# Kernel optimization log

Measured on AMD Instinct MI355X. Metric: run time of the kernel, lower is better.

## Reference

```python
import jax, jax.numpy as jnp
import numpy as np

B, S, D_IN, D_OUT, E = 4, 2048, 1024, 1024, 8

def setup_inputs() -> dict:
    key = jax.random.key(0)
    ks = jax.random.split(key, 5)
    scale = 1.0 / np.sqrt(D_IN)
    x  = jax.random.normal(ks[0], (B, S, D_IN), dtype=jnp.float32)
    We = jax.random.uniform(ks[1], (E, D_OUT, D_IN), dtype=jnp.float32, minval=-scale, maxval=scale)
    be = jax.random.uniform(ks[2], (E, D_OUT), dtype=jnp.float32, minval=-scale, maxval=scale)
    Wg = jax.random.uniform(ks[3], (E, D_IN), dtype=jnp.float32, minval=-scale, maxval=scale)
    bg = jax.random.uniform(ks[4], (E,), dtype=jnp.float32, minval=-scale, maxval=scale)
    return {"x": x, "We": We, "be": be, "Wg": Wg, "bg": bg}

def reference(x, We, be, Wg, bg):
    # gate: [B,S,E]
    gate_logits = jnp.einsum('bsd,ed->bse', x, Wg) + bg
    gate = jax.nn.softmax(gate_logits, axis=-1)
    top1 = jnp.argmax(gate, axis=-1)                      # [B,S]
    one_hot = jax.nn.one_hot(top1, E, dtype=x.dtype)      # [B,S,E]
    # all-expert dense outputs, stacked on last axis: [B,S,O,E]
    expert_outs = jnp.einsum('bsd,eod->bsoe', x, We) + be.T
    out = jnp.einsum('bsoe,bse->bso', expert_outs, one_hot)
    mean_gate = gate.mean(axis=(0, 1))                    # [E]
    aux_loss = jnp.mean((mean_gate * E) ** 2)
    return (out, aux_loss)
```

## Files before the change

kernel.cpp:

```cpp
#include <hip/hip_runtime.h>
#include <hip/hip_bf16.h>


#define NTOK 8192
#define DIN  1024
#define DOUT 1024
#define NE   8

typedef unsigned short u16;
typedef unsigned int   u32;
typedef unsigned long long u64;
typedef short  bf16x8 __attribute__((ext_vector_type(8)));
typedef float  f32x4  __attribute__((ext_vector_type(4)));

__device__ __forceinline__ u16 f2bf(float f) {
    __hip_bfloat16 h = __float2bfloat16(f);
    return *(u16*)&h;
}


__global__ __launch_bounds__(256) void gate_kernel(
    const float* __restrict__ x, const float* __restrict__ Wg,
    const float* __restrict__ bg, u32* __restrict__ stage)
{
    __shared__ int   am_s[16];
    __shared__ float mg_s[4][NE];

    const int tid  = threadIdx.x;
    const int wave = tid >> 6;
    const int lane = tid & 63;
    const int g    = lane >> 3;
    const int sub  = lane & 7;

    const float* wr = Wg + g * DIN + 4 * sub;

    float bgl[NE];
    #pragma unroll
    for (int e = 0; e < NE; ++e) bgl[e] = bg[e];

    float mgacc = 0.f;

    #pragma unroll 1
    for (int it = 0; it < 4; ++it) {
        const int t = blockIdx.x * 16 + wave * 4 + it;
        const float* xr = x + (size_t)t * DIN + 4 * sub;

        float acc0 = 0.f, acc1 = 0.f, acc2 = 0.f, acc3 = 0.f;
        #pragma unroll
        for (int j = 0; j < 8; ++j) {
            const int k = j * 128;
            f32x4 x0 = *(const f32x4*)(xr + k);
            f32x4 w0 = *(const f32x4*)(wr + k);
            f32x4 x1 = *(const f32x4*)(xr + k + 32);
            f32x4 w1 = *(const f32x4*)(wr + k + 32);
            f32x4 x2 = *(const f32x4*)(xr + k + 64);
            f32x4 w2 = *(const f32x4*)(wr + k + 64);
            f32x4 x3 = *(const f32x4*)(xr + k + 96);
            f32x4 w3 = *(const f32x4*)(wr + k + 96);
            #pragma unroll
            for (int q = 0; q < 4; ++q) {
                acc0 = fmaf(w0[q], x0[q], acc0);
                acc1 = fmaf(w1[q], x1[q], acc1);
                acc2 = fmaf(w2[q], x2[q], acc2);
                acc3 = fmaf(w3[q], x3[q], acc3);
            }
        }
        float acc = (acc0 + acc1) + (acc2 + acc3);

        acc += __shfl_xor(acc, 1, 64);
        acc += __shfl_xor(acc, 2, 64);
        acc += __shfl_xor(acc, 4, 64);

        float logit[NE];
        #pragma unroll
        for (int e = 0; e < NE; ++e)
            logit[e] = __shfl(acc, e * 8, 64) + bgl[e];

        float m = logit[0]; int am = 0;
        #pragma unroll
        for (int e = 1; e < NE; ++e) if (logit[e] > m) { m = logit[e]; am = e; }

        float p[NE], s = 0.f;
        #pragma unroll
        for (int e = 0; e < NE; ++e) { p[e] = __expf(logit[e] - m); s += p[e]; }
        const float inv = 1.f / s;

        float psel = p[0];
        #pragma unroll
        for (int e = 1; e < NE; ++e) psel = (lane == e) ? p[e] : psel;
        if (lane < NE) mgacc += psel * inv;

        if (lane == 0) am_s[wave * 4 + it] = am;
    }

    if (lane < NE) mg_s[wave][lane] = mgacc;
    __syncthreads();

    u32* rec = stage + (size_t)blockIdx.x * 16;
    if (tid == 0) {
        u64 pack = 0;
        #pragma unroll
        for (int i = 0; i < 16; ++i) pack |= (u64)am_s[i] << (4 * i);
        *(u64*)rec = pack;
    }
    if (tid < NE) {
        float s = mg_s[0][tid] + mg_s[1][tid] + mg_s[2][tid] + mg_s[3][tid];
        rec[2 + tid] = __float_as_uint(s);
    }
}

__global__ __launch_bounds__(512) void route_kernel(
    const u32* __restrict__ stage, int* __restrict__ counts,
    int* __restrict__ tok_list, float* __restrict__ out)
{
    __shared__ float mgl[512][NE];
    __shared__ int   c[512][9];
    __shared__ float tot_s[NE];

    const int tid  = threadIdx.x;
    const int wave = tid >> 6;
    const int lane = tid & 63;

    const u64 pack = *(const u64*)(stage + (size_t)tid * 16);
    #pragma unroll
    for (int e = 0; e < NE; ++e)
        mgl[tid][e] = __uint_as_float(stage[tid * 16 + 2 + e]);

    #pragma unroll
    for (int e = 0; e < 9; ++e) c[tid][e] = 0;

    #pragma unroll
    for (int it = 0; it < 16; ++it) {
        int e3 = (int)((pack >> (4 * it)) & 7);
        c[tid][e3]++;
    }
    __syncthreads();

    {
        const int e = wave;
        int carry = 0;
        #pragma unroll 1
        for (int ch = 0; ch < 8; ++ch) {
            int v = c[ch * 64 + lane][e];
            int incl = v;
            #pragma unroll
            for (int off = 1; off < 64; off <<= 1) {
                int n = __shfl_up(incl, off, 64);
                if (lane >= off) incl += n;
            }
            c[ch * 64 + lane][e] = incl - v + carry;
            carry += __shfl(incl, 63, 64);
        }
        if (lane == 0) counts[e] = carry;
    }
    __syncthreads();

    #pragma unroll
    for (int it = 0; it < 16; ++it) {
        int e3 = (int)((pack >> (4 * it)) & 7);
        int pos = c[tid][e3]++;
        tok_list[e3 * NTOK + pos] = tid * 16 + it;
    }

    {
        const int e = wave;
        float s = 0.f;
        #pragma unroll
        for (int ch = 0; ch < 8; ++ch) s += mgl[ch * 64 + lane][e];
        #pragma unroll
        for (int off = 32; off > 0; off >>= 1) s += __shfl_xor(s, off, 64);
        if (lane == 0) tot_s[e] = s;
    }
    __syncthreads();
    if (tid == 0) {
        float s = 0.f;
        #pragma unroll
        for (int e = 0; e < NE; ++e) {
            float m = tot_s[e] * (8.0f / 8192.0f);
            s += m * m;
        }
        out[(size_t)NTOK * DOUT] = s * 0.125f;
    }
}

__global__ __launch_bounds__(256) void moe_gemm(
    const float* __restrict__ x, const float* __restrict__ We,
    const float* __restrict__ be, const int* __restrict__ counts,
    const int* __restrict__ tok_list, float* __restrict__ out)
{
    const int e   = blockIdx.z;
    const int cnt = counts[e];
    const int m0  = blockIdx.y * 128;
    if (m0 >= cnt) return;
    const int n0  = blockIdx.x * 128;

    __shared__ u16 sA[128 * 32];
    __shared__ u16 sB[128 * 32];
    __shared__ int toks[128];

    const int tid = threadIdx.x;
    if (tid < 128) {
        int gr = m0 + tid;
        toks[tid] = (gr < cnt) ? tok_list[e * NTOK + gr] : tok_list[e * NTOK];
    }
    __syncthreads();

    const int lane = tid & 63;
    const int wave = tid >> 6;
    const int wm   = (wave & 1) * 64;
    const int wn   = (wave >> 1) * 64;
    const int lrow = lane & 15;
    const int quad = lane >> 4;

    f32x4 acc[4][4];
    #pragma unroll
    for (int i = 0; i < 4; ++i)
        #pragma unroll
        for (int j = 0; j < 4; ++j) acc[i][j] = (f32x4){0.f, 0.f, 0.f, 0.f};

    const int srow  = tid >> 1;
    const int shalf = (tid & 1) * 16;

    const float* xrow = x  + (size_t)toks[srow] * DIN + shalf;
    const float* brow = We + ((size_t)e << 20) + ((size_t)(n0 + srow) << 10) + shalf;

    #pragma unroll 1
    for (int k0 = 0; k0 < DIN; k0 += 32) {
        f32x4 a[4], b[4];
        #pragma unroll
        for (int q = 0; q < 4; ++q) {
            a[q] = *(const f32x4*)(xrow + k0 + 4 * q);
            b[q] = *(const f32x4*)(brow + k0 + 4 * q);
        }
        union { u16 h[16]; uint4 u[2]; } pa, pb;
        #pragma unroll
        for (int q = 0; q < 4; ++q)
            #pragma unroll
            for (int j = 0; j < 4; ++j) {
                pa.h[q * 4 + j] = f2bf(a[q][j]);
                pb.h[q * 4 + j] = f2bf(b[q][j]);
            }
        *(uint4*)&sA[srow * 32 + shalf]     = pa.u[0];
        *(uint4*)&sA[srow * 32 + shalf + 8] = pa.u[1];
        *(uint4*)&sB[srow * 32 + shalf]     = pb.u[0];
        *(uint4*)&sB[srow * 32 + shalf + 8] = pb.u[1];
        __syncthreads();

        bf16x8 af[4], bfr[4];
        #pragma unroll
        for (int i = 0; i < 4; ++i)
            af[i] = *(const bf16x8*)&sA[(wm + i * 16 + lrow) * 32 + quad * 8];
        #pragma unroll
        for (int j = 0; j < 4; ++j)
            bfr[j] = *(const bf16x8*)&sB[(wn + j * 16 + lrow) * 32 + quad * 8];
        #pragma unroll
        for (int i = 0; i < 4; ++i)
            #pragma unroll
            for (int j = 0; j < 4; ++j)
                acc[i][j] = __builtin_amdgcn_mfma_f32_16x16x32_bf16(
                    af[i], bfr[j], acc[i][j], 0, 0, 0);
        __syncthreads();
    }

    #pragma unroll
    for (int j = 0; j < 4; ++j) {
        const int col = n0 + wn + j * 16 + lrow;
        const float bev = be[e * DOUT + col];
        #pragma unroll
        for (int i = 0; i < 4; ++i) {
            #pragma unroll
            for (int r = 0; r < 4; ++r) {
                const int rl = wm + i * 16 + quad * 4 + r;
                if (m0 + rl < cnt) {
                    const int tok = toks[rl];
                    out[((size_t)tok << 10) + col] = acc[i][j][r] + bev;
                }
            }
        }
    }
}

extern "C" void kernel_launch(void* const* d_in, const int* in_sizes, int n_in,
                              void* d_out, int out_size, void* d_ws, size_t ws_size,
                              hipStream_t stream) {
    const float* x  = (const float*)d_in[0];
    const float* We = (const float*)d_in[1];
    const float* be = (const float*)d_in[2];
    const float* Wg = (const float*)d_in[3];
    const float* bg = (const float*)d_in[4];
    float* out = (float*)d_out;

    int* counts   = (int*)d_ws;
    int* tok_list = (int*)((char*)d_ws + 256);
    u32* stage    = (u32*)((char*)d_ws + 256);

    gate_kernel<<<512, 256, 0, stream>>>(x, Wg, bg, stage);
    route_kernel<<<1, 512, 0, stream>>>(stage, counts, tok_list, out);
    moe_gemm<<<dim3(8, 64, 8), 256, 0, stream>>>(x, We, be, counts, tok_list, out);
}
```

Baseline: 187.0 us.

## Double K-tile to 64 with XOR-swizzled LDS and flattened expert-major grid

Result: slower. 276.2 us (+47.7%).

```diff
diff --git a/kernel.cpp b/kernel.cpp
--- a/kernel.cpp
+++ b/kernel.cpp
@@ -188,14 +188,15 @@
     const float* __restrict__ be, const int* __restrict__ counts,
     const int* __restrict__ tok_list, float* __restrict__ out)
 {
-    const int e   = blockIdx.z;
+    const int d  = blockIdx.x;
+    const int e  = (d >> 6) & 7;
     const int cnt = counts[e];
-    const int m0  = blockIdx.y * 128;
+    const int m0 = (d & 63) * 128;
     if (m0 >= cnt) return;
-    const int n0  = blockIdx.x * 128;
-
-    __shared__ u16 sA[128 * 32];
-    __shared__ u16 sB[128 * 32];
+    const int n0 = (d >> 9) * 128;
+
+    __shared__ u16 sA[128 * 64];
+    __shared__ u16 sB[128 * 64];
     __shared__ int toks[128];
 
     const int tid = threadIdx.x;
@@ -218,47 +219,65 @@
         #pragma unroll
         for (int j = 0; j < 4; ++j) acc[i][j] = (f32x4){0.f, 0.f, 0.f, 0.f};
 
-    const int srow  = tid >> 1;
-    const int shalf = (tid & 1) * 16;
-
-    const float* xrow = x  + (size_t)toks[srow] * DIN + shalf;
-    const float* brow = We + ((size_t)e << 20) + ((size_t)(n0 + srow) << 10) + shalf;
+    const int t3 = tid >> 3;
+    const int ch = tid & 7;
+    const int cx = ch ^ (t3 & 7);
+
+    const float* aP[4];
+    const float* bP[4];
+    #pragma unroll
+    for (int p = 0; p < 4; ++p) {
+        const int r = p * 32 + t3;
+        aP[p] = x  + (size_t)toks[r] * DIN + ch * 8;
+        bP[p] = We + ((size_t)e << 20) + ((size_t)(n0 + r) << 10) + ch * 8;
+    }
+
+    const int l7 = lrow & 7;
 
     #pragma unroll 1
-    for (int k0 = 0; k0 < DIN; k0 += 32) {
-        f32x4 a[4], b[4];
-        #pragma unroll
-        for (int q = 0; q < 4; ++q) {
-            a[q] = *(const f32x4*)(xrow + k0 + 4 * q);
-            b[q] = *(const f32x4*)(brow + k0 + 4 * q);
-        }
-        union { u16 h[16]; uint4 u[2]; } pa, pb;
-        #pragma unroll
-        for (int q = 0; q < 4; ++q)
-            #pragma unroll
-            for (int j = 0; j < 4; ++j) {
-                pa.h[q * 4 + j] = f2bf(a[q][j]);
-                pb.h[q * 4 + j] = f2bf(b[q][j]);
-            }
-        *(uint4*)&sA[srow * 32 + shalf]     = pa.u[0];
-        *(uint4*)&sA[srow * 32 + shalf + 8] = pa.u[1];
-        *(uint4*)&sB[srow * 32 + shalf]     = pb.u[0];
-        *(uint4*)&sB[srow * 32 + shalf + 8] = pb.u[1];
+    for (int k0 = 0; k0 < DIN; k0 += 64) {
+        f32x4 a0[4], a1[4], b0[4], b1[4];
+        #pragma unroll
+        for (int p = 0; p < 4; ++p) {
+            a0[p] = *(const f32x4*)(aP[p] + k0);
+            a1[p] = *(const f32x4*)(aP[p] + k0 + 4);
+            b0[p] = *(const f32x4*)(bP[p] + k0);
+            b1[p] = *(const f32x4*)(bP[p] + k0 + 4);
+        }
+        #pragma unroll
+        for (int p = 0; p < 4; ++p) {
+            union { u16 h[8]; uint4 u; } ua, ub;
+            #pragma unroll
+            for (int q = 0; q < 4; ++q) {
+                ua.h[q]     = f2bf(a0[p][q]);
+                ua.h[4 + q] = f2bf(a1[p][q]);
+                ub.h[q]     = f2bf(b0[p][q]);
+                ub.h[4 + q] = f2bf(b1[p][q]);
+            }
+            const int r = p * 32 + t3;
+            *(uint4*)&sA[r * 64 + cx * 8] = ua.u;
+            *(uint4*)&sB[r * 64 + cx * 8] = ub.u;
+        }
         __syncthreads();
 
-        bf16x8 af[4], bfr[4];
-        #pragma unroll
-        for (int i = 0; i < 4; ++i)
-            af[i] = *(const bf16x8*)&sA[(wm + i * 16 + lrow) * 32 + quad * 8];
-        #pragma unroll
-        for (int j = 0; j < 4; ++j)
-            bfr[j] = *(const bf16x8*)&sB[(wn + j * 16 + lrow) * 32 + quad * 8];
-        #pragma unroll
-        for (int i = 0; i < 4; ++i)
-            #pragma unroll
-            for (int j = 0; j < 4; ++j)
-                acc[i][j] = __builtin_amdgcn_mfma_f32_16x16x32_bf16(
-                    af[i], bfr[j], acc[i][j], 0, 0, 0);
+        bf16x8 af[2][4], bfr[2][4];
+        #pragma unroll
+        for (int ks = 0; ks < 2; ++ks) {
+            const int so = ((ks * 4 + quad) ^ l7) * 8;
+            #pragma unroll
+            for (int i = 0; i < 4; ++i) {
+                af[ks][i]  = *(const bf16x8*)&sA[(wm + i * 16 + lrow) * 64 + so];
+                bfr[ks][i] = *(const bf16x8*)&sB[(wn + i * 16 + lrow) * 64 + so];
+            }
+        }
+        #pragma unroll
+        for (int ks = 0; ks < 2; ++ks)
+            #pragma unroll
+            for (int i = 0; i < 4; ++i)
+                #pragma unroll
+                for (int j = 0; j < 4; ++j)
+                    acc[i][j] = __builtin_amdgcn_mfma_f32_16x16x32_bf16(
+                        af[ks][i], bfr[ks][j], acc[i][j], 0, 0, 0);
         __syncthreads();
     }
 
@@ -296,5 +315,5 @@
 
     gate_kernel<<<512, 256, 0, stream>>>(x, Wg, bg, stage);
     route_kernel<<<1, 512, 0, stream>>>(stage, counts, tok_list, out);
-    moe_gemm<<<dim3(8, 64, 8), 256, 0, stream>>>(x, We, be, counts, tok_list, out);
-}
+    moe_gemm<<<4096, 256, 0, stream>>>(x, We, be, counts, tok_list, out);
+}
```

## Replace LDS-staged GEMM with single-wave register-direct tiles and double-buffered loads

Applied to the files above, without the earlier changes.

Result: slower. 284.4 us (+52.1%).

```diff
diff --git a/kernel.cpp b/kernel.cpp
--- a/kernel.cpp
+++ b/kernel.cpp
@@ -183,98 +183,110 @@
     }
 }
 
-__global__ __launch_bounds__(256) void moe_gemm(
+__global__ __launch_bounds__(64) void moe_gemm(
     const float* __restrict__ x, const float* __restrict__ We,
     const float* __restrict__ be, const int* __restrict__ counts,
     const int* __restrict__ tok_list, float* __restrict__ out)
 {
-    const int e   = blockIdx.z;
+    const int d   = blockIdx.x;
+    const int mlo = d & 7;
+    const int n   = (d >> 3) & 15;
+    const int e   = (d >> 7) & 7;
+    const int mhi = d >> 10;
     const int cnt = counts[e];
-    const int m0  = blockIdx.y * 128;
+    const int m0  = (mlo + 8 * mhi) * 64;
     if (m0 >= cnt) return;
-    const int n0  = blockIdx.x * 128;
-
-    __shared__ u16 sA[128 * 32];
-    __shared__ u16 sB[128 * 32];
-    __shared__ int toks[128];
-
-    const int tid = threadIdx.x;
-    if (tid < 128) {
-        int gr = m0 + tid;
-        toks[tid] = (gr < cnt) ? tok_list[e * NTOK + gr] : tok_list[e * NTOK];
-    }
-    __syncthreads();
-
-    const int lane = tid & 63;
-    const int wave = tid >> 6;
-    const int wm   = (wave & 1) * 64;
-    const int wn   = (wave >> 1) * 64;
+    const int n0  = n * 64;
+
+    const int lane = threadIdx.x;
     const int lrow = lane & 15;
     const int quad = lane >> 4;
 
+    int atok[4];
+    #pragma unroll
+    for (int i = 0; i < 4; ++i) {
+        int gr = m0 + i * 16 + lrow;
+        atok[i] = tok_list[e * NTOK + (gr < cnt ? gr : cnt - 1)];
+    }
+
+    const float* aP[4];
+    const float* bP[4];
+    #pragma unroll
+    for (int i = 0; i < 4; ++i)
+        aP[i] = x + (size_t)atok[i] * DIN + quad * 8;
+    #pragma unroll
+    for (int j = 0; j < 4; ++j)
+        bP[j] = We + ((size_t)e << 20) + ((size_t)(n0 + j * 16 + lrow) << 10) + quad * 8;
+
     f32x4 acc[4][4];
     #pragma unroll
     for (int i = 0; i < 4; ++i)
         #pragma unroll
         for (int j = 0; j < 4; ++j) acc[i][j] = (f32x4){0.f, 0.f, 0.f, 0.f};
 
-    const int srow  = tid >> 1;
-    const int shalf = (tid & 1) * 16;
-
-    const float* xrow = x  + (size_t)toks[srow] * DIN + shalf;
-    const float* brow = We + ((size_t)e << 20) + ((size_t)(n0 + srow) << 10) + shalf;
-
+    f32x4 A0[8], B0[8], A1[8], B1[8];
+
+    #define LD(Ab, Bb, k0)                                       \
+        do {                                                     \
+            _Pragma("unroll")                                    \
+            for (int i = 0; i < 4; ++i) {                        \
+                Ab[2*i]   = *(const f32x4*)(aP[i] + (k0));       \
+                Ab[2*i+1] = *(const f32x4*)(aP[i] + (k0) + 4);   \
+                Bb[2*i]   = *(const f32x4*)(bP[i] + (k0));       \
+                Bb[2*i+1] = *(const f32x4*)(bP[i] + (k0) + 4);   \
+            }                                                    \
+        } while (0)
+
+    #define CP(Ab, Bb)                                                        \
+        do {                                                                  \
+            bf16x8 af[4], bf[4];                                              \
+            _Pragma("unroll")                                                 \
+            for (int i = 0; i < 4; ++i) {                                     \
+                union { u16 h[8]; bf16x8 v; } ua, ub;                         \
+                _Pragma("unroll")                                             \
+                for (int q = 0; q < 4; ++q) {                                 \
+                    ua.h[q]     = f2bf(Ab[2*i][q]);                           \
+                    ua.h[4 + q] = f2bf(Ab[2*i+1][q]);                         \
+                    ub.h[q]     = f2bf(Bb[2*i][q]);                           \
+                    ub.h[4 + q] = f2bf(Bb[2*i+1][q]);                         \
+                }                                                             \
+                af[i] = ua.v; bf[i] = ub.v;                                   \
+            }                                                                 \
+            _Pragma("unroll")                                                 \
+            for (int i = 0; i < 4; ++i)                                       \
+                _Pragma("unroll")                                             \
+                for (int j = 0; j < 4; ++j)                                   \
+                    acc[i][j] = __builtin_amdgcn_mfma_f32_16x16x32_bf16(      \
+                        af[i], bf[j], acc[i][j], 0, 0, 0);                    \
+        } while (0)
+
+    LD(A0, B0, 0);
     #pragma unroll 1
-    for (int k0 = 0; k0 < DIN; k0 += 32) {
-        f32x4 a[4], b[4];
-        #pragma unroll
-        for (int q = 0; q < 4; ++q) {
-            a[q] = *(const f32x4*)(xrow + k0 + 4 * q);
-            b[q] = *(const f32x4*)(brow + k0 + 4 * q);
-        }
-        union { u16 h[16]; uint4 u[2]; } pa, pb;
-        #pragma unroll
-        for (int q = 0; q < 4; ++q)
-            #pragma unroll
-            for (int j = 0; j < 4; ++j) {
-                pa.h[q * 4 + j] = f2bf(a[q][j]);
-                pb.h[q * 4 + j] = f2bf(b[q][j]);
-            }
-        *(uint4*)&sA[srow * 32 + shalf]     = pa.u[0];
-        *(uint4*)&sA[srow * 32 + shalf + 8] = pa.u[1];
-        *(uint4*)&sB[srow * 32 + shalf]     = pb.u[0];
-        *(uint4*)&sB[srow * 32 + shalf + 8] = pb.u[1];
-        __syncthreads();
-
-        bf16x8 af[4], bfr[4];
-        #pragma unroll
-        for (int i = 0; i < 4; ++i)
-            af[i] = *(const bf16x8*)&sA[(wm + i * 16 + lrow) * 32 + quad * 8];
-        #pragma unroll
-        for (int j = 0; j < 4; ++j)
-            bfr[j] = *(const bf16x8*)&sB[(wn + j * 16 + lrow) * 32 + quad * 8];
-        #pragma unroll
-        for (int i = 0; i < 4; ++i)
-            #pragma unroll
-            for (int j = 0; j < 4; ++j)
-                acc[i][j] = __builtin_amdgcn_mfma_f32_16x16x32_bf16(
-                    af[i], bfr[j], acc[i][j], 0, 0, 0);
-        __syncthreads();
-    }
+    for (int k0 = 0; k0 <= DIN - 128; k0 += 64) {
+        LD(A1, B1, k0 + 32);
+        CP(A0, B0);
+        LD(A0, B0, k0 + 64);
+        CP(A1, B1);
+    }
+    LD(A1, B1, DIN - 32);
+    CP(A0, B0);
+    CP(A1, B1);
+
+    #undef LD
+    #undef CP
 
     #pragma unroll
     for (int j = 0; j < 4; ++j) {
-        const int col = n0 + wn + j * 16 + lrow;
+        const int col = n0 + j * 16 + lrow;
         const float bev = be[e * DOUT + col];
         #pragma unroll
         for (int i = 0; i < 4; ++i) {
             #pragma unroll
             for (int r = 0; r < 4; ++r) {
-                const int rl = wm + i * 16 + quad * 4 + r;
-                if (m0 + rl < cnt) {
-                    const int tok = toks[rl];
+                const int rl = m0 + i * 16 + quad * 4 + r;
+                const int tok = __shfl(atok[i], quad * 4 + r, 64);
+                if (rl < cnt)
                     out[((size_t)tok << 10) + col] = acc[i][j][r] + bev;
-                }
             }
         }
     }
@@ -296,5 +308,5 @@
 
     gate_kernel<<<512, 256, 0, stream>>>(x, Wg, bg, stage);
     route_kernel<<<1, 512, 0, stream>>>(stage, counts, tok_list, out);
-    moe_gemm<<<dim3(8, 64, 8), 256, 0, stream>>>(x, We, be, counts, tok_list, out);
-}
+    moe_gemm<<<4096, 64, 0, stream>>>(x, We, be, counts, tok_list, out);
+}
```

## Double-buffer MoE GEMM tiles via direct global-to-LDS loads with swizzle

Applied to the files above, without the earlier changes.

Measured after the change: 201.5 us. 1.08x slower.

```diff
diff --git a/kernel.cpp b/kernel.cpp
--- a/kernel.cpp
+++ b/kernel.cpp
@@ -17,6 +17,11 @@
     __hip_bfloat16 h = __float2bfloat16(f);
     return *(u16*)&h;
 }
+
+#define GLDS16(g, l)                                                  \
+    __builtin_amdgcn_global_load_lds(                                 \
+        (__attribute__((address_space(1))) void*)(g),                 \
+        (__attribute__((address_space(3))) void*)(l), 16, 0, 0)
 
 
 __global__ __launch_bounds__(256) void gate_kernel(
@@ -194,8 +199,8 @@
     if (m0 >= cnt) return;
     const int n0  = blockIdx.x * 128;
 
-    __shared__ u16 sA[128 * 32];
-    __shared__ u16 sB[128 * 32];
+    __shared__ float sA[2][128 * 32];
+    __shared__ float sB[2][128 * 32];
     __shared__ int toks[128];
 
     const int tid = threadIdx.x;
@@ -211,6 +216,19 @@
     const int wn   = (wave >> 1) * 64;
     const int lrow = lane & 15;
     const int quad = lane >> 4;
+    const int l7   = lrow & 7;
+
+    const int ro  = lane >> 3;
+    const int csw = (lane & 7) ^ ro;
+
+    const float* aSrc[4];
+    const float* bSrc[4];
+    #pragma unroll
+    for (int i = 0; i < 4; ++i) {
+        const int r = wave * 32 + i * 8 + ro;
+        aSrc[i] = x + (size_t)toks[r] * DIN + csw * 4;
+        bSrc[i] = We + ((size_t)e << 20) + ((size_t)(n0 + r) << 10) + csw * 4;
+    }
 
     f32x4 acc[4][4];
     #pragma unroll
@@ -218,49 +236,60 @@
         #pragma unroll
         for (int j = 0; j < 4; ++j) acc[i][j] = (f32x4){0.f, 0.f, 0.f, 0.f};
 
-    const int srow  = tid >> 1;
-    const int shalf = (tid & 1) * 16;
-
-    const float* xrow = x  + (size_t)toks[srow] * DIN + shalf;
-    const float* brow = We + ((size_t)e << 20) + ((size_t)(n0 + srow) << 10) + shalf;
-
+    #define STAGE(buf, k0)                                               \
+        do {                                                             \
+            _Pragma("unroll")                                            \
+            for (int i = 0; i < 4; ++i) {                                \
+                GLDS16(aSrc[i] + (k0), &sA[buf][(wave * 32 + i * 8) * 32]); \
+                GLDS16(bSrc[i] + (k0), &sB[buf][(wave * 32 + i * 8) * 32]); \
+            }                                                            \
+        } while (0)
+
+    #define COMPUTE(buf)                                                      \
+        do {                                                                  \
+            bf16x8 af[4], bv[4];                                              \
+            _Pragma("unroll")                                                 \
+            for (int i = 0; i < 4; ++i) {                                     \
+                const int ra = (wm + i * 16 + lrow) * 32;                     \
+                const int rb = (wn + i * 16 + lrow) * 32;                     \
+                f32x4 a0 = *(const f32x4*)&sA[buf][ra + (((2*quad)  ^l7)<<2)];\
+                f32x4 a1 = *(const f32x4*)&sA[buf][ra + (((2*quad+1)^l7)<<2)];\
+                f32x4 b0 = *(const f32x4*)&sB[buf][rb + (((2*quad)  ^l7)<<2)];\
+                f32x4 b1 = *(const f32x4*)&sB[buf][rb + (((2*quad+1)^l7)<<2)];\
+                union { u16 h[8]; bf16x8 v; } ua, ub;                         \
+                _Pragma("unroll")                                             \
+                for (int q = 0; q < 4; ++q) {                                 \
+                    ua.h[q]     = f2bf(a0[q]);                                \
+                    ua.h[4 + q] = f2bf(a1[q]);                                \
+                    ub.h[q]     = f2bf(b0[q]);                                \
+                    ub.h[4 + q] = f2bf(b1[q]);                                \
+                }                                                             \
+                af[i] = ua.v; bv[i] = ub.v;                                   \
+            }                                                                 \
+            _Pragma("unroll")                                                 \
+            for (int i = 0; i < 4; ++i)                                       \
+                _Pragma("unroll")                                             \
+                for (int j = 0; j < 4; ++j)                                   \
+                    acc[i][j] = __builtin_amdgcn_mfma_f32_16x16x32_bf16(      \
+                        af[i], bv[j], acc[i][j], 0, 0, 0);                    \
+        } while (0)
+
+    STAGE(0, 0);
+    asm volatile("s_waitcnt vmcnt(0)" ::: "memory");
+    __builtin_amdgcn_s_barrier();
+
+    int buf = 0;
     #pragma unroll 1
     for (int k0 = 0; k0 < DIN; k0 += 32) {
-        f32x4 a[4], b[4];
-        #pragma unroll
-        for (int q = 0; q < 4; ++q) {
-            a[q] = *(const f32x4*)(xrow + k0 + 4 * q);
-            b[q] = *(const f32x4*)(brow + k0 + 4 * q);
-        }
-        union { u16 h[16]; uint4 u[2]; } pa, pb;
-        #pragma unroll
-        for (int q = 0; q < 4; ++q)
-            #pragma unroll
-            for (int j = 0; j < 4; ++j) {
-                pa.h[q * 4 + j] = f2bf(a[q][j]);
-                pb.h[q * 4 + j] = f2bf(b[q][j]);
-            }
-        *(uint4*)&sA[srow * 32 + shalf]     = pa.u[0];
-        *(uint4*)&sA[srow * 32 + shalf + 8] = pa.u[1];
-        *(uint4*)&sB[srow * 32 + shalf]     = pb.u[0];
-        *(uint4*)&sB[srow * 32 + shalf + 8] = pb.u[1];
-        __syncthreads();
-
-        bf16x8 af[4], bfr[4];
-        #pragma unroll
-        for (int i = 0; i < 4; ++i)
-            af[i] = *(const bf16x8*)&sA[(wm + i * 16 + lrow) * 32 + quad * 8];
-        #pragma unroll
-        for (int j = 0; j < 4; ++j)
-            bfr[j] = *(const bf16x8*)&sB[(wn + j * 16 + lrow) * 32 + quad * 8];
-        #pragma unroll
-        for (int i = 0; i < 4; ++i)
-            #pragma unroll
-            for (int j = 0; j < 4; ++j)
-                acc[i][j] = __builtin_amdgcn_mfma_f32_16x16x32_bf16(
-                    af[i], bfr[j], acc[i][j], 0, 0, 0);
-        __syncthreads();
-    }
+        if (k0 + 32 < DIN) STAGE(buf ^ 1, k0 + 32);
+        COMPUTE(buf);
+        asm volatile("s_waitcnt vmcnt(0)" ::: "memory");
+        __builtin_amdgcn_s_barrier();
+        buf ^= 1;
+    }
+
+    #undef STAGE
+    #undef COMPUTE
 
     #pragma unroll
     for (int j = 0; j < 4; ++j) {
```
